# Kernel tuning notes

Measured on AMD Instinct MI355X. Metric: run time of the kernel, lower is better.

The kernel has to match this reference:

```python
import jax, jax.numpy as jnp
import numpy as np

D_MODEL = 256
HIDDEN = 64
R = 1            # corr_radius
MAX_DELTA = 4.0  # max_delta_px
GROUPS = 8       # _gn_groups(64)
B, H, W = 2, 128, 128


def grid_sample_border(img, grid):
    """Bilinear grid_sample, padding_mode='border', align_corners=False.
    img: [B,C,H,W], grid: [B,Hg,Wg,2] (x,y in [-1,1]-ish). -> [B,C,Hg,Wg]"""
    Bi, C, Hi, Wi = img.shape
    x = (grid[..., 0] + 1.0) * (Wi * 0.5) - 0.5
    y = (grid[..., 1] + 1.0) * (Hi * 0.5) - 0.5
    x = jnp.clip(x, 0.0, Wi - 1.0)
    y = jnp.clip(y, 0.0, Hi - 1.0)
    x0 = jnp.floor(x); y0 = jnp.floor(y)
    wx = (x - x0)[:, None]; wy = (y - y0)[:, None]
    x0i = x0.astype(jnp.int32); y0i = y0.astype(jnp.int32)
    x1i = jnp.minimum(x0i + 1, Wi - 1); y1i = jnp.minimum(y0i + 1, Hi - 1)
    imgf = img.reshape(Bi, C, Hi * Wi)
    def gat(im, yi, xi):  # im [C,HW], yi/xi [Hg,Wg]
        return im[:, (yi * Wi + xi).reshape(-1)].reshape(C, *yi.shape)
    g = jax.vmap(gat)
    v00 = g(imgf, y0i, x0i); v01 = g(imgf, y0i, x1i)
    v10 = g(imgf, y1i, x0i); v11 = g(imgf, y1i, x1i)
    return (v00 * (1 - wx) * (1 - wy) + v01 * wx * (1 - wy)
            + v10 * (1 - wx) * wy + v11 * wx * wy)


def l2norm(x, axis):
    n = jnp.sqrt(jnp.sum(x * x, axis=axis, keepdims=True))
    return x / jnp.maximum(n, 1e-12)


def conv2d(x, w, pad):
    return jax.lax.conv_general_dilated(x, w, (1, 1), [(pad, pad), (pad, pad)],
                                        dimension_numbers=('NCHW', 'OIHW', 'NCHW'))


def group_norm(x, gamma, beta, groups=GROUPS, eps=1e-5):
    Bi, C, Hi, Wi = x.shape
    xg = x.reshape(Bi, groups, C // groups, Hi, Wi)
    mu = xg.mean(axis=(2, 3, 4), keepdims=True)
    var = xg.var(axis=(2, 3, 4), keepdims=True)
    xn = ((xg - mu) * jax.lax.rsqrt(var + eps)).reshape(Bi, C, Hi, Wi)
    return xn * gamma[None, :, None, None] + beta[None, :, None, None]


def conv_gn_gelu(x, w, g, b, pad):
    return jax.nn.gelu(group_norm(conv2d(x, w, pad), g, b), approximate=False)


def make_grid(h, w):
    xs = (jnp.arange(w, dtype=jnp.float32) + 0.5) * (2.0 / w) - 1.0
    ys = (jnp.arange(h, dtype=jnp.float32) + 0.5) * (2.0 / h) - 1.0
    gx, gy = jnp.meshgrid(xs, ys, indexing='xy')
    return jnp.stack([gx, gy], axis=-1)[None]  # [1,H,W,2]


def setup_inputs() -> dict:
    key = jax.random.key(0)
    ks = jax.random.split(key, 12)
    in_ch = D_MODEL * 3 + 2 + 1 + (2 * R + 1) ** 2  # 780
    def w(k, o, i, kh, kw):
        return (jax.random.normal(k, (o, i, kh, kw), jnp.float32)
                / np.sqrt(i * kh * kw).astype(np.float32))
    return {
        'feat_A_map': jax.random.normal(ks[0], (B, D_MODEL, H, W), jnp.float32),
        'feat_B_map': jax.random.normal(ks[1], (B, D_MODEL, H, W), jnp.float32),
        'coarse_warp': jax.random.uniform(ks[2], (B, H, W, 2), jnp.float32, -1.0, 1.0),
        'confidence': jax.random.uniform(ks[3], (B, H, W), jnp.float32),
        'enc1_w': w(ks[4], HIDDEN, in_ch, 1, 1),
        'gn1_g': jnp.ones(HIDDEN, jnp.float32), 'gn1_b': jnp.zeros(HIDDEN, jnp.float32),
        'enc2_w': w(ks[5], HIDDEN, HIDDEN, 3, 3),
        'gn2_g': jnp.ones(HIDDEN, jnp.float32), 'gn2_b': jnp.zeros(HIDDEN, jnp.float32),
        'enc3_w': w(ks[6], HIDDEN, HIDDEN, 3, 3),
        'gn3_g': jnp.ones(HIDDEN, jnp.float32), 'gn3_b': jnp.zeros(HIDDEN, jnp.float32),
        'delta_w': w(ks[7], 2, HIDDEN, 3, 3) * 0.01, 'delta_b': jnp.zeros(2, jnp.float32),
        'conf_w': w(ks[8], 1, HIDDEN, 3, 3) * 0.01, 'conf_b': jnp.zeros(1, jnp.float32),
    }


def reference(feat_A_map, feat_B_map, coarse_warp, confidence,
              enc1_w, gn1_g, gn1_b, enc2_w, gn2_g, gn2_b, enc3_w, gn3_g, gn3_b,
              delta_w, delta_b, conf_w, conf_b):
    cw = jnp.clip(jnp.nan_to_num(coarse_warp, nan=0.0, posinf=1.5, neginf=-1.5), -1.5, 1.5)
    route = jax.lax.stop_gradient(cw)  # detached routing warp
    warped_B = grid_sample_border(feat_B_map, route)
    src = make_grid(H, W)
    disp = jnp.transpose(cw - src, (0, 3, 1, 2))  # [B,2,H,W]
    conf = jnp.clip(jnp.nan_to_num(confidence, nan=0.0, posinf=1.0, neginf=0.0), 0.0, 1.0)
    conf_chw = conf[:, None]
    # warp-aware correlation over (2R+1)^2 offsets, vectorized via vmap
    fa_n = l2norm(jnp.nan_to_num(feat_A_map, nan=0.0, posinf=0.0, neginf=0.0), axis=1)
    fb = jnp.nan_to_num(feat_B_map, nan=0.0, posinf=0.0, neginf=0.0)
    offs = jnp.asarray([[2.0 * dx / W, 2.0 * dy / H]
                        for dy in range(-R, R + 1) for dx in range(-R, R + 1)],
                       dtype=jnp.float32)  # [K,2]
    grids = jnp.clip(jnp.nan_to_num(route[None] + offs[:, None, None, None, :],
                                    nan=0.0, posinf=1.5, neginf=-1.5), -1.5, 1.5)
    sampled = jax.vmap(grid_sample_border, in_axes=(None, 0))(fb, grids)  # [K,B,C,H,W]
    corr = jnp.transpose(jnp.sum(fa_n[None] * l2norm(sampled, axis=2), axis=2),
                         (1, 0, 2, 3))  # [B,K,H,W]
    x = jnp.concatenate([feat_A_map, warped_B, jnp.abs(feat_A_map - warped_B),
                         disp, conf_chw, corr], axis=1)
    h = conv_gn_gelu(x, enc1_w, gn1_g, gn1_b, 0)
    h = conv_gn_gelu(h, enc2_w, gn2_g, gn2_b, 1)
    h = conv_gn_gelu(h, enc3_w, gn3_g, gn3_b, 1)
    delta_raw = jnp.transpose(jnp.tanh(conv2d(h, delta_w, 1)
                                       + delta_b[None, :, None, None]), (0, 2, 3, 1))
    scale = jnp.asarray([2.0 * MAX_DELTA / W, 2.0 * MAX_DELTA / H], jnp.float32)
    fine_warp = jnp.clip(jnp.nan_to_num(route + delta_raw * scale,
                                        nan=0.0, posinf=1.5, neginf=-1.5), -1.5, 1.5)
    conf_delta = (conv2d(h, conf_w, 1) + conf_b[None, :, None, None])[:, 0]
    p = jnp.clip(conf, 1e-4, 1.0 - 1e-4)
    base_logit = jnp.log(p) - jnp.log1p(-p)
    refined_logits = base_logit + 0.5 * conf_delta
    refined_conf = jnp.clip(jax.nn.sigmoid(refined_logits), 0.0, 1.0)
    return (fine_warp, refined_conf, refined_logits)
```

## Files before the change

kernel.cpp:

```cpp
#include <hip/hip_runtime.h>
#include <hip/hip_bf16.h>
#include <math.h>

#define B_ 2
#define H_ 128
#define W_ 128
#define C_ 256
#define HID 64
#define PIX_PER (H_*W_)
#define NPIX (B_*PIX_PER)
#define K1STEPS 25
#define K3STEPS 18
#define SROW 264

using f32x4 = __attribute__((ext_vector_type(4))) float;
using s16x8 = __attribute__((ext_vector_type(8))) short;
using u16x2 = __attribute__((ext_vector_type(2))) unsigned short;
using u16x4 = __attribute__((ext_vector_type(4))) unsigned short;
using u16x8 = __attribute__((ext_vector_type(8))) unsigned short;

__device__ __forceinline__ float bf2f(unsigned short u) {
    return __uint_as_float(((unsigned)u) << 16);
}
__device__ __forceinline__ unsigned short f2bf(float f) {
    unsigned u = __float_as_uint(f);
    u += 0x7FFFu + ((u >> 16) & 1u);
    return (unsigned short)(u >> 16);
}
__device__ __forceinline__ float clean15(float v) {
    if (v != v) v = 0.f;
    return fminf(fmaxf(v, -1.5f), 1.5f);
}
__device__ __forceinline__ float clean01(float v) {
    if (v != v) v = 0.f;
    return fminf(fmaxf(v, 0.f), 1.f);
}

__global__ __launch_bounds__(256) void k_transpose(const float* __restrict__ A,
                                                   const float* __restrict__ Bm,
                                                   unsigned short* __restrict__ faT,
                                                   unsigned short* __restrict__ fbT,
                                                   const float* __restrict__ w1,
                                                   const float* __restrict__ w2,
                                                   const float* __restrict__ w3,
                                                   unsigned short* __restrict__ p1,
                                                   unsigned short* __restrict__ p2,
                                                   unsigned short* __restrict__ p3)
{
    if (blockIdx.z == 4) {
        if (blockIdx.y != 0 || blockIdx.x >= 61) return;
        int t = blockIdx.x * 256 + threadIdx.x;
        if (t < 6400) {
            int lane = t & 63, nt = (t >> 6) & 3, ks = t >> 8;
            int n = nt * 16 + (lane & 15);
            int kb = ks * 32 + 8 * (lane >> 4);
#pragma unroll
            for (int j = 0; j < 8; j++) {
                int k = kb + j;
                p1[(size_t)t * 8 + j] = (k < 780) ? f2bf(w1[(size_t)n * 780 + k]) : (unsigned short)0;
            }
        } else if (t < 6400 + 2 * 4608) {
            int which = (t - 6400) / 4608;
            int idx = (t - 6400) % 4608;
            const float* w = which ? w3 : w2;
            unsigned short* p = which ? p3 : p2;
            int lane = idx & 63, nt = (idx >> 6) & 3, ks = idx >> 8;
            int n = nt * 16 + (lane & 15);
            int tap = ks >> 1;
            int ky = tap / 3, kx = tap % 3;
#pragma unroll
            for (int j = 0; j < 8; j++) {
                int c = (ks & 1) * 32 + 8 * (lane >> 4) + j;
                p[(size_t)idx * 8 + j] = f2bf(w[(((size_t)n * 64 + c) * 3 + ky) * 3 + kx]);
            }
        }
        return;
    }
    __shared__ float tile[32][33];
    int hw0 = blockIdx.x * 32;
    int c0  = blockIdx.y * 32;
    int z   = blockIdx.z;
    int b   = z >> 1;
    const float* src = (z & 1) ? Bm : A;
    unsigned short* dst = (z & 1) ? fbT : faT;
    int tx = threadIdx.x & 31, ty = threadIdx.x >> 5;
    const float* s = src + ((size_t)b * C_ + c0) * (size_t)PIX_PER + hw0;
#pragma unroll
    for (int i = 0; i < 32; i += 8) {
        float v = s[(size_t)(ty + i) * PIX_PER + tx];
        if (!isfinite(v)) v = 0.f;
        tile[ty + i][tx] = v;
    }
    __syncthreads();
    unsigned short* d = dst + ((size_t)b * PIX_PER + hw0) * C_ + c0;
    int pr = threadIdx.x & 15;
    int hw = threadIdx.x >> 4;
#pragma unroll
    for (int i = 0; i < 32; i += 16) {
        int hwl = hw + i;
        u16x2 o;
        o[0] = f2bf(tile[2 * pr][hwl]);
        o[1] = f2bf(tile[2 * pr + 1][hwl]);
        *(u16x2*)(d + (size_t)hwl * C_ + 2 * pr) = o;
    }
}

__global__ __launch_bounds__(256) void k_sample(const float* __restrict__ cw,
                                                const float* __restrict__ confp,
                                                const unsigned short* __restrict__ faT,
                                                const unsigned short* __restrict__ fbT,
                                                unsigned short* __restrict__ wbbuf,
                                                unsigned short* __restrict__ tail)
{
    __shared__ unsigned short S[4][17 * SROW];
    __shared__ float CT[4][16 * 20 + 4];
    int lane = threadIdx.x & 63;
    int wv = threadIdx.x >> 6;
    int wid = blockIdx.x * 4 + wv;
    int b = wid >> 14, y = (wid >> 7) & 127, x = wid & 127;

    float gx = clean15(cw[(size_t)wid * 2 + 0]);
    float gy = clean15(cw[(size_t)wid * 2 + 1]);
    float conf = clean01(confp[wid]);

    float pxu = (gx + 1.f) * 64.f - 0.5f;
    float pyu = (gy + 1.f) * 64.f - 0.5f;
    float x0f = floorf(pxu), y0f = floorf(pyu);
    float wx = pxu - x0f, wy = pyu - y0f;
    int x0 = (int)x0f, y0 = (int)y0f;
    int co[4], ro[4];
#pragma unroll
    for (int k = 0; k < 4; k++) {
        co[k] = min(max(x0 - 1 + k, 0), 127) << 8;
        ro[k] = min(max(y0 - 1 + k, 0), 127) << 15;
    }
    const unsigned short* fbP = fbT + ((size_t)b << 22);

    int h = lane >> 5, lo = lane & 31;
    u16x8 stg[8];
#pragma unroll
    for (int i = 0; i < 8; i++) {
        int rr = ro[i >> 1];
        int cc = h ? co[((i & 1) << 1) + 1] : co[(i & 1) << 1];
        stg[i] = *(const u16x8*)(fbP + rr + cc + lo * 8);
    }
    u16x8 stfa;
    if (h == 0) stfa = *(const u16x8*)(faT + (size_t)wid * C_ + lo * 8);

    unsigned short* Sw = &S[wv][0];
#pragma unroll
    for (int i = 0; i < 8; i++)
        *(u16x8*)(Sw + (2 * i + h) * SROW + lo * 8) = stg[i];
    if (h == 0) *(u16x8*)(Sw + 16 * SROW + lo * 8) = stfa;

    int q = lane & 15;
    int tA = (q == 0) ? 16 : q - 1;
    int koff = (lane >> 4) * 8;
    const unsigned short* pA = Sw + tA * SROW + koff;
    const unsigned short* pB = Sw + q * SROW + koff;
    f32x4 acc = {0.f, 0.f, 0.f, 0.f};
#pragma unroll
    for (int ks = 0; ks < 8; ks++) {
        s16x8 av = *(const s16x8*)(pA + ks * 32);
        s16x8 bv = *(const s16x8*)(pB + ks * 32);
        acc = __builtin_amdgcn_mfma_f32_16x16x32_bf16(av, bv, acc, 0, 0, 0);
    }
    *(f32x4*)&CT[wv][q * 20 + (lane >> 4) * 4] = acc;

    float w00 = (1.f - wx) * (1.f - wy), w01 = wx * (1.f - wy);
    float w10 = (1.f - wx) * wy,         w11 = wx * wy;
    u16x4 v5  = *(const u16x4*)(Sw + 5 * SROW + lane * 4);
    u16x4 v6  = *(const u16x4*)(Sw + 6 * SROW + lane * 4);
    u16x4 v9  = *(const u16x4*)(Sw + 9 * SROW + lane * 4);
    u16x4 v10 = *(const u16x4*)(Sw + 10 * SROW + lane * 4);
    u16x4 v15 = *(const u16x4*)(Sw + 15 * SROW + lane * 4);
    u16x4 vfa = *(const u16x4*)(Sw + 16 * SROW + lane * 4);
    float fa2p = 0.f, t152p = 0.f;
    u16x4 wbo;
#pragma unroll
    for (int i = 0; i < 4; i++) {
        float s = w00 * bf2f(v5[i]) + w01 * bf2f(v6[i])
                + w10 * bf2f(v9[i]) + w11 * bf2f(v10[i]);
        wbo[i] = f2bf(s);
        float fv = bf2f(vfa[i]), tv = bf2f(v15[i]);
        fa2p  += fv * fv;
        t152p += tv * tv;
    }
    *(u16x4*)(wbbuf + (size_t)wid * C_ + lane * 4) = wbo;
#pragma unroll
    for (int m = 1; m < 64; m <<= 1) {
        fa2p  += __shfl_xor(fa2p, m);
        t152p += __shfl_xor(t152p, m);
    }

    if (lane < 32) {
        float outv = 0.f;
        if (lane == 0)      outv = gx - (((float)x + 0.5f) * 0.015625f - 1.f);
        else if (lane == 1) outv = gy - (((float)y + 0.5f) * 0.015625f - 1.f);
        else if (lane == 2) outv = conf;
        else if (lane < 12) {
            int j = lane - 3;
            int jd = j / 3, jm = j - jd * 3;
            int m00 = jd * 4 + jm;
            const float* Cw = &CT[wv][0];
            float D00 = Cw[m00 * 20], D01 = Cw[(m00 + 1) * 20];
            float D10 = Cw[(m00 + 4) * 20], D11 = Cw[(m00 + 5) * 20];
            float dot = w00 * D00 + w01 * D01 + w10 * D10 + w11 * D11;
#define GR(a, b) Cw[(b) * 20 + (a) + 1]
            float g11 = (j == 8) ? t152p : GR(m00 + 5, m00 + 5);
            float s2 = w00 * w00 * GR(m00, m00) + w01 * w01 * GR(m00 + 1, m00 + 1)
                     + w10 * w10 * GR(m00 + 4, m00 + 4) + w11 * w11 * g11
                     + 2.f * (w00 * w01 * GR(m00, m00 + 1) + w00 * w10 * GR(m00, m00 + 4)
                            + w00 * w11 * GR(m00, m00 + 5) + w01 * w10 * GR(m00 + 1, m00 + 4)
                            + w01 * w11 * GR(m00 + 1, m00 + 5) + w10 * w11 * GR(m00 + 4, m00 + 5));
#undef GR
            outv = dot * rsqrtf(fmaxf(fa2p, 1e-24f)) * rsqrtf(fmaxf(s2, 1e-24f));
        }
        tail[(size_t)wid * 32 + lane] = f2bf(outv);
    }
}

__device__ __forceinline__ void gn_epilogue(const f32x4 acc[4], float* lds,
                                            float* __restrict__ pbuf, int bid,
                                            int la, int lb, int wv)
{
    int d = la >> 3;
    int slot = wv * 32 + lb * 8 + (la & 7);
#pragma unroll
    for (int nt = 0; nt < 4; nt++) {
        float s  = acc[nt][0] + acc[nt][1] + acc[nt][2] + acc[nt][3];
        float s2 = acc[nt][0] * acc[nt][0] + acc[nt][1] * acc[nt][1]
                 + acc[nt][2] * acc[nt][2] + acc[nt][3] * acc[nt][3];
        int g = nt * 2 + d;
        lds[(g * 128 + slot) * 2 + 0] = s;
        lds[(g * 128 + slot) * 2 + 1] = s2;
    }
    __syncthreads();
    int tid = threadIdx.x;
    int g = tid >> 5, i = tid & 31;
    float s  = lds[(g * 128 + i) * 2]     + lds[(g * 128 + i + 32) * 2]
             + lds[(g * 128 + i + 64) * 2] + lds[(g * 128 + i + 96) * 2];
    float s2 = lds[(g * 128 + i) * 2 + 1]     + lds[(g * 128 + i + 32) * 2 + 1]
             + lds[(g * 128 + i + 64) * 2 + 1] + lds[(g * 128 + i + 96) * 2 + 1];
#pragma unroll
    for (int m = 1; m < 32; m <<= 1) { s += __shfl_xor(s, m); s2 += __shfl_xor(s2, m); }
    if (i == 0) {
        pbuf[(bid * 8 + g) * 2]     = s;
        pbuf[(bid * 8 + g) * 2 + 1] = s2;
    }
}

__global__ __launch_bounds__(256) void k_gemm1(const unsigned short* __restrict__ faT,
                                               const unsigned short* __restrict__ wbbuf,
                                               const unsigned short* __restrict__ tail,
                                               const unsigned short* __restrict__ pack,
                                               unsigned short* __restrict__ hpre,
                                               float* __restrict__ pbuf)
{
    __shared__ float lds[8 * 128 * 2];
    int wave = (blockIdx.x * 256 + threadIdx.x) >> 6;
    int lane = threadIdx.x & 63;
    int la = lane & 15, lb = lane >> 4;
    int row = wave * 16 + la;
    const unsigned short* fa_row = faT   + (size_t)row * C_ + lb * 8;
    const unsigned short* wb_row = wbbuf + (size_t)row * C_ + lb * 8;
    f32x4 acc[4] = {{0,0,0,0},{0,0,0,0},{0,0,0,0},{0,0,0,0}};

#pragma unroll
    for (int ks = 0; ks < 8; ks++) {
        s16x8 a = *(const s16x8*)(fa_row + ks * 32);
#pragma unroll
        for (int nt = 0; nt < 4; nt++)
            acc[nt] = __builtin_amdgcn_mfma_f32_16x16x32_bf16(a,
                *(const s16x8*)(pack + ((size_t)(ks * 4 + nt) * 64 + lane) * 8), acc[nt], 0, 0, 0);
    }
#pragma unroll
    for (int ks = 0; ks < 8; ks++) {
        s16x8 a = *(const s16x8*)(wb_row + ks * 32);
#pragma unroll
        for (int nt = 0; nt < 4; nt++)
            acc[nt] = __builtin_amdgcn_mfma_f32_16x16x32_bf16(a,
                *(const s16x8*)(pack + ((size_t)((ks + 8) * 4 + nt) * 64 + lane) * 8), acc[nt], 0, 0, 0);
    }
#pragma unroll
    for (int ks = 0; ks < 8; ks++) {
        u16x8 av = *(const u16x8*)(fa_row + ks * 32);
        u16x8 bv = *(const u16x8*)(wb_row + ks * 32);
        s16x8 a;
#pragma unroll
        for (int j = 0; j < 8; j++)
            a[j] = (short)f2bf(fabsf(bf2f(av[j]) - bf2f(bv[j])));
#pragma unroll
        for (int nt = 0; nt < 4; nt++)
            acc[nt] = __builtin_amdgcn_mfma_f32_16x16x32_bf16(a,
                *(const s16x8*)(pack + ((size_t)((ks + 16) * 4 + nt) * 64 + lane) * 8), acc[nt], 0, 0, 0);
    }
    {
        s16x8 a = *(const s16x8*)(tail + (size_t)row * 32 + lb * 8);
#pragma unroll
        for (int nt = 0; nt < 4; nt++)
            acc[nt] = __builtin_amdgcn_mfma_f32_16x16x32_bf16(a,
                *(const s16x8*)(pack + ((size_t)(24 * 4 + nt) * 64 + lane) * 8), acc[nt], 0, 0, 0);
    }

    int orow = wave * 16 + lb * 4;
#pragma unroll
    for (int nt = 0; nt < 4; nt++)
#pragma unroll
        for (int r = 0; r < 4; r++)
            hpre[(size_t)(orow + r) * HID + nt * 16 + la] = f2bf(acc[nt][r]);

    gn_epilogue(acc, lds, pbuf, blockIdx.x, la, lb, (threadIdx.x >> 6));
}

__global__ __launch_bounds__(256) void k_conv3(const unsigned short* __restrict__ hin,
                                               const unsigned short* __restrict__ pack,
                                               unsigned short* __restrict__ hpre,
                                               float* __restrict__ pbuf)
{
    __shared__ float lds[8 * 128 * 2];
    int wave = (blockIdx.x * 256 + threadIdx.x) >> 6;
    int lane = threadIdx.x & 63;
    int la = lane & 15, lb = lane >> 4;
    int b = wave >> 10, y = (wave >> 3) & 127, xb = (wave & 7) * 16;
    int xx = xb + la;
    f32x4 acc[4] = {{0,0,0,0},{0,0,0,0},{0,0,0,0},{0,0,0,0}};
#pragma unroll
    for (int ks = 0; ks < K3STEPS; ks++) {
        int tap = ks >> 1;
        int yy = y + tap / 3 - 1;
        int xq = xx + tap % 3 - 1;
        s16x8 a = {0,0,0,0,0,0,0,0};
        if ((unsigned)yy < 128u && (unsigned)xq < 128u)
            a = *(const s16x8*)(hin + ((size_t)((b * 128 + yy) * 128 + xq)) * HID
                                + (ks & 1) * 32 + lb * 8);
#pragma unroll
        for (int nt = 0; nt < 4; nt++)
            acc[nt] = __builtin_amdgcn_mfma_f32_16x16x32_bf16(a,
                *(const s16x8*)(pack + ((size_t)(ks * 4 + nt) * 64 + lane) * 8), acc[nt], 0, 0, 0);
    }
    int orow = wave * 16 + lb * 4;
#pragma unroll
    for (int nt = 0; nt < 4; nt++)
#pragma unroll
        for (int r = 0; r < 4; r++)
            hpre[(size_t)(orow + r) * HID + nt * 16 + la] = f2bf(acc[nt][r]);

    gn_epilogue(acc, lds, pbuf, blockIdx.x, la, lb, (threadIdx.x >> 6));
}

__global__ __launch_bounds__(256) void k_gnapply(const unsigned short* __restrict__ hpre,
                                                 const float* __restrict__ gamma,
                                                 const float* __restrict__ beta,
                                                 const float* __restrict__ pbuf,
                                                 unsigned short* __restrict__ hn)
{
    int pix0 = blockIdx.x * 32;
    int b = pix0 >> 14;
    __shared__ float sm[16];
    {
        int g = threadIdx.x >> 5, i = threadIdx.x & 31;
        float s = 0.f, s2 = 0.f;
#pragma unroll
        for (int k = 0; k < 8; k++) {
            int bid = b * 256 + i + k * 32;
            s  += pbuf[(bid * 8 + g) * 2];
            s2 += pbuf[(bid * 8 + g) * 2 + 1];
        }
#pragma unroll
        for (int m = 1; m < 32; m <<= 1) { s += __shfl_xor(s, m); s2 += __shfl_xor(s2, m); }
        if (i == 0) {
            const float inv = 1.f / 131072.f;
            float mean = s * inv;
            float var = fmaxf(s2 * inv - mean * mean, 0.f);
            sm[g * 2] = mean;
            sm[g * 2 + 1] = rsqrtf(var + 1e-5f);
        }
    }
    __syncthreads();
    int t = blockIdx.x * 256 + threadIdx.x;
    int pix = t >> 3, g = t & 7;
    float mean = sm[g * 2], rstd = sm[g * 2 + 1];
    u16x8 v = *(const u16x8*)(hpre + (size_t)pix * HID + g * 8);
    u16x8 o;
#pragma unroll
    for (int i = 0; i < 8; i++) {
        int c = g * 8 + i;
        float xn = (bf2f(v[i]) - mean) * rstd * gamma[c] + beta[c];
        float ge = 0.5f * xn * (1.f + erff(xn * 0.70710678118654752f));
        o[i] = f2bf(ge);
    }
    *(u16x8*)(hn + (size_t)pix * HID + g * 8) = o;
}

__global__ __launch_bounds__(256) void k_final(const unsigned short* __restrict__ hn,
                                               const float* __restrict__ cw,
                                               const float* __restrict__ confp,
                                               const float* __restrict__ dw,
                                               const float* __restrict__ db,
                                               const float* __restrict__ cwgt,
                                               const float* __restrict__ cb,
                                               float* __restrict__ out)
{
    __shared__ float wds[1154];
    __shared__ float wcs[577];
    int tid = threadIdx.x;
    for (int i = tid; i < 1152; i += 256) wds[i] = dw[i];
    for (int i = tid; i < 576; i += 256) wcs[i] = cwgt[i];
    if (tid == 0) { wds[1152] = db[0]; wds[1153] = db[1]; wcs[576] = cb[0]; }
    __syncthreads();

    int t = blockIdx.x * 256 + tid;
    int pix = t >> 3, part = t & 7;
    int b = pix >> 14, y = (pix >> 7) & 127, x = pix & 127;

    float d0 = 0.f, d1 = 0.f, c0 = 0.f;
#pragma unroll
    for (int ky = 0; ky < 3; ky++) {
        int yy = y + ky - 1;
        if ((unsigned)yy >= 128u) continue;
#pragma unroll
        for (int kx = 0; kx < 3; kx++) {
            int xq = x + kx - 1;
            if ((unsigned)xq >= 128u) continue;
            const unsigned short* hp = hn + (size_t)((b * 128 + yy) * 128 + xq) * HID + part * 8;
            int widx = ky * 3 + kx;
            u16x8 v = *(const u16x8*)hp;
#pragma unroll
            for (int i = 0; i < 8; i++) {
                float f = bf2f(v[i]);
                int c = part * 8 + i;
                d0 += f * wds[c * 9 + widx];
                d1 += f * wds[576 + c * 9 + widx];
                c0 += f * wcs[c * 9 + widx];
            }
        }
    }
#pragma unroll
    for (int m = 1; m < 8; m <<= 1) {
        d0 += __shfl_xor(d0, m);
        d1 += __shfl_xor(d1, m);
        c0 += __shfl_xor(c0, m);
    }
    if (part == 0) {
        d0 = tanhf(d0 + wds[1152]);
        d1 = tanhf(d1 + wds[1153]);
        c0 += wcs[576];

        float gx = clean15(cw[(size_t)pix * 2 + 0]);
        float gy = clean15(cw[(size_t)pix * 2 + 1]);
        float fwx = fminf(fmaxf(gx + d0 * 0.0625f, -1.5f), 1.5f);
        float fwy = fminf(fmaxf(gy + d1 * 0.0625f, -1.5f), 1.5f);

        float conf = clean01(confp[pix]);
        float p = fminf(fmaxf(conf, 1e-4f), 1.f - 1e-4f);
        float bl = logf(p) - log1pf(-p);
        float rl = bl + 0.5f * c0;
        float rc = fminf(fmaxf(1.f / (1.f + expf(-rl)), 0.f), 1.f);

        out[(size_t)pix * 2 + 0] = fwx;
        out[(size_t)pix * 2 + 1] = fwy;
        out[(size_t)NPIX * 2 + pix] = rc;
        out[(size_t)NPIX * 2 + NPIX + pix] = rl;
    }
}

extern "C" void kernel_launch(void* const* d_in, const int* in_sizes, int n_in,
                              void* d_out, int out_size, void* d_ws, size_t ws_size,
                              hipStream_t stream)
{
    const float* feat_A = (const float*)d_in[0];
    const float* feat_B = (const float*)d_in[1];
    const float* cw     = (const float*)d_in[2];
    const float* conf   = (const float*)d_in[3];
    const float* w1     = (const float*)d_in[4];
    const float* g1     = (const float*)d_in[5];
    const float* b1     = (const float*)d_in[6];
    const float* w2     = (const float*)d_in[7];
    const float* g2     = (const float*)d_in[8];
    const float* b2     = (const float*)d_in[9];
    const float* w3     = (const float*)d_in[10];
    const float* g3     = (const float*)d_in[11];
    const float* b3     = (const float*)d_in[12];
    const float* dw     = (const float*)d_in[13];
    const float* db     = (const float*)d_in[14];
    const float* cwgt   = (const float*)d_in[15];
    const float* cb     = (const float*)d_in[16];
    float* out = (float*)d_out;

    char* w = (char*)d_ws;
    size_t o = 0;
    unsigned short* faT  = (unsigned short*)(w + o); o += (size_t)NPIX * C_ * 2;
    unsigned short* fbT  = (unsigned short*)(w + o); o += (size_t)NPIX * C_ * 2;
    unsigned short* wbb  = (unsigned short*)(w + o); o += (size_t)NPIX * C_ * 2;
    unsigned short* tail = (unsigned short*)(w + o); o += (size_t)NPIX * 32 * 2;
    unsigned short* hpre = (unsigned short*)(w + o); o += (size_t)NPIX * HID * 2;
    unsigned short* hnA  = (unsigned short*)(w + o); o += (size_t)NPIX * HID * 2;
    unsigned short* hnB  = (unsigned short*)(w + o); o += (size_t)NPIX * HID * 2;
    unsigned short* p1   = (unsigned short*)(w + o); o += (size_t)K1STEPS * 4 * 64 * 8 * 2;
    unsigned short* p2   = (unsigned short*)(w + o); o += (size_t)K3STEPS * 4 * 64 * 8 * 2;
    unsigned short* p3   = (unsigned short*)(w + o); o += (size_t)K3STEPS * 4 * 64 * 8 * 2;
    float* pbuf = (float*)(w + o);

    k_transpose<<<dim3(PIX_PER / 32, C_ / 32, 5), 256, 0, stream>>>(feat_A, feat_B, faT, fbT,
                                                                    w1, w2, w3, p1, p2, p3);
    k_sample<<<NPIX / 4, 256, 0, stream>>>(cw, conf, faT, fbT, wbb, tail);

    k_gemm1<<<(NPIX / 16) / 4, 256, 0, stream>>>(faT, wbb, tail, p1, hpre, pbuf);
    k_gnapply<<<NPIX / 32, 256, 0, stream>>>(hpre, g1, b1, pbuf, hnA);

    k_conv3<<<(NPIX / 16) / 4, 256, 0, stream>>>(hnA, p2, hpre, pbuf);
    k_gnapply<<<NPIX / 32, 256, 0, stream>>>(hpre, g2, b2, pbuf, hnB);

    k_conv3<<<(NPIX / 16) / 4, 256, 0, stream>>>(hnB, p3, hpre, pbuf);
    k_gnapply<<<NPIX / 32, 256, 0, stream>>>(hpre, g3, b3, pbuf, hnA);

    k_final<<<NPIX * 8 / 256, 256, 0, stream>>>(hnA, cw, conf, dw, db, cwgt, cb, out);
}
```

Baseline: 140.2 us.

## Fuse sampling/correlation kernel with first encoder GEMM through shared memory

Merges the bilinear sampling and correlation kernel with the first 1x1 conv GEMM. Each block now samples 16 pixels (four per wave) and stages the concatenated feature row (feat_A, warped_B, |diff|, tail) in LDS, then runs the GEMM directly from LDS. This removes the global round trip of the warped_B and tail buffers and the separate re-read of feat_A, and computes |diff| once per element. In exchange LDS use per block grows, each wave does four sequential sampling iterations with a block barrier, GN partial sums now come from 1024 blocks per batch (gnapply gets a blocks-per-batch parameter), and the first GEMM is split with one 16-column N tile per wave instead of four per wave.

Measured after the change: 147.9 us. +5.5%, slower.

```diff
diff --git a/kernel.cpp b/kernel.cpp
--- a/kernel.cpp
+++ b/kernel.cpp
@@ -12,6 +12,7 @@
 #define K1STEPS 25
 #define K3STEPS 18
 #define SROW 264
+#define AROW 808
 
 using f32x4 = __attribute__((ext_vector_type(4))) float;
 using s16x8 = __attribute__((ext_vector_type(8))) short;
@@ -105,118 +106,157 @@
     }
 }
 
-__global__ __launch_bounds__(256) void k_sample(const float* __restrict__ cw,
-                                                const float* __restrict__ confp,
-                                                const unsigned short* __restrict__ faT,
-                                                const unsigned short* __restrict__ fbT,
-                                                unsigned short* __restrict__ wbbuf,
-                                                unsigned short* __restrict__ tail)
-{
+__global__ __launch_bounds__(256) void k_samgemm(const float* __restrict__ cw,
+                                                 const float* __restrict__ confp,
+                                                 const unsigned short* __restrict__ faT,
+                                                 const unsigned short* __restrict__ fbT,
+                                                 const unsigned short* __restrict__ pack,
+                                                 unsigned short* __restrict__ hpre,
+                                                 float* __restrict__ pbuf)
+{
+    __shared__ unsigned short Ap[16 * AROW];
     __shared__ unsigned short S[4][17 * SROW];
     __shared__ float CT[4][16 * 20 + 4];
     int lane = threadIdx.x & 63;
     int wv = threadIdx.x >> 6;
-    int wid = blockIdx.x * 4 + wv;
-    int b = wid >> 14, y = (wid >> 7) & 127, x = wid & 127;
-
-    float gx = clean15(cw[(size_t)wid * 2 + 0]);
-    float gy = clean15(cw[(size_t)wid * 2 + 1]);
-    float conf = clean01(confp[wid]);
-
-    float pxu = (gx + 1.f) * 64.f - 0.5f;
-    float pyu = (gy + 1.f) * 64.f - 0.5f;
-    float x0f = floorf(pxu), y0f = floorf(pyu);
-    float wx = pxu - x0f, wy = pyu - y0f;
-    int x0 = (int)x0f, y0 = (int)y0f;
-    int co[4], ro[4];
-#pragma unroll
-    for (int k = 0; k < 4; k++) {
-        co[k] = min(max(x0 - 1 + k, 0), 127) << 8;
-        ro[k] = min(max(y0 - 1 + k, 0), 127) << 15;
-    }
-    const unsigned short* fbP = fbT + ((size_t)b << 22);
-
-    int h = lane >> 5, lo = lane & 31;
-    u16x8 stg[8];
-#pragma unroll
-    for (int i = 0; i < 8; i++) {
-        int rr = ro[i >> 1];
-        int cc = h ? co[((i & 1) << 1) + 1] : co[(i & 1) << 1];
-        stg[i] = *(const u16x8*)(fbP + rr + cc + lo * 8);
-    }
-    u16x8 stfa;
-    if (h == 0) stfa = *(const u16x8*)(faT + (size_t)wid * C_ + lo * 8);
-
     unsigned short* Sw = &S[wv][0];
-#pragma unroll
-    for (int i = 0; i < 8; i++)
-        *(u16x8*)(Sw + (2 * i + h) * SROW + lo * 8) = stg[i];
-    if (h == 0) *(u16x8*)(Sw + 16 * SROW + lo * 8) = stfa;
-
-    int q = lane & 15;
-    int tA = (q == 0) ? 16 : q - 1;
-    int koff = (lane >> 4) * 8;
-    const unsigned short* pA = Sw + tA * SROW + koff;
-    const unsigned short* pB = Sw + q * SROW + koff;
+
+#pragma unroll
+    for (int it = 0; it < 4; it++) {
+        int prow = wv * 4 + it;
+        int wid = blockIdx.x * 16 + prow;
+        int b = wid >> 14, y = (wid >> 7) & 127, x = wid & 127;
+
+        float gx = clean15(cw[(size_t)wid * 2 + 0]);
+        float gy = clean15(cw[(size_t)wid * 2 + 1]);
+        float conf = clean01(confp[wid]);
+
+        float pxu = (gx + 1.f) * 64.f - 0.5f;
+        float pyu = (gy + 1.f) * 64.f - 0.5f;
+        float x0f = floorf(pxu), y0f = floorf(pyu);
+        float wx = pxu - x0f, wy = pyu - y0f;
+        int x0 = (int)x0f, y0 = (int)y0f;
+        int co[4], ro[4];
+#pragma unroll
+        for (int k = 0; k < 4; k++) {
+            co[k] = min(max(x0 - 1 + k, 0), 127) << 8;
+            ro[k] = min(max(y0 - 1 + k, 0), 127) << 15;
+        }
+        const unsigned short* fbP = fbT + ((size_t)b << 22);
+
+        int h = lane >> 5, lo = lane & 31;
+        u16x8 stg[8];
+#pragma unroll
+        for (int i = 0; i < 8; i++) {
+            int rr = ro[i >> 1];
+            int cc = h ? co[((i & 1) << 1) + 1] : co[(i & 1) << 1];
+            stg[i] = *(const u16x8*)(fbP + rr + cc + lo * 8);
+        }
+        u16x8 stfa;
+        if (h == 0) stfa = *(const u16x8*)(faT + (size_t)wid * C_ + lo * 8);
+#pragma unroll
+        for (int i = 0; i < 8; i++)
+            *(u16x8*)(Sw + (2 * i + h) * SROW + lo * 8) = stg[i];
+        if (h == 0) *(u16x8*)(Sw + 16 * SROW + lo * 8) = stfa;
+
+        int q = lane & 15;
+        int tA = (q == 0) ? 16 : q - 1;
+        int koff = (lane >> 4) * 8;
+        const unsigned short* pA = Sw + tA * SROW + koff;
+        const unsigned short* pB = Sw + q * SROW + koff;
+        f32x4 acc = {0.f, 0.f, 0.f, 0.f};
+#pragma unroll
+        for (int ks = 0; ks < 8; ks++) {
+            s16x8 av = *(const s16x8*)(pA + ks * 32);
+            s16x8 bv = *(const s16x8*)(pB + ks * 32);
+            acc = __builtin_amdgcn_mfma_f32_16x16x32_bf16(av, bv, acc, 0, 0, 0);
+        }
+        *(f32x4*)&CT[wv][q * 20 + (lane >> 4) * 4] = acc;
+
+        float w00 = (1.f - wx) * (1.f - wy), w01 = wx * (1.f - wy);
+        float w10 = (1.f - wx) * wy,         w11 = wx * wy;
+        u16x4 v5  = *(const u16x4*)(Sw + 5 * SROW + lane * 4);
+        u16x4 v6  = *(const u16x4*)(Sw + 6 * SROW + lane * 4);
+        u16x4 v9  = *(const u16x4*)(Sw + 9 * SROW + lane * 4);
+        u16x4 v10 = *(const u16x4*)(Sw + 10 * SROW + lane * 4);
+        u16x4 v15 = *(const u16x4*)(Sw + 15 * SROW + lane * 4);
+        u16x4 vfa = *(const u16x4*)(Sw + 16 * SROW + lane * 4);
+        float fa2p = 0.f, t152p = 0.f;
+        u16x4 wbo, dfo;
+#pragma unroll
+        for (int i = 0; i < 4; i++) {
+            float s = w00 * bf2f(v5[i]) + w01 * bf2f(v6[i])
+                    + w10 * bf2f(v9[i]) + w11 * bf2f(v10[i]);
+            float fv = bf2f(vfa[i]), tv = bf2f(v15[i]);
+            wbo[i] = f2bf(s);
+            dfo[i] = f2bf(fabsf(fv - s));
+            fa2p  += fv * fv;
+            t152p += tv * tv;
+        }
+        unsigned short* Ar = &Ap[prow * AROW];
+        *(u16x4*)(Ar + lane * 4)       = vfa;
+        *(u16x4*)(Ar + 256 + lane * 4) = wbo;
+        *(u16x4*)(Ar + 512 + lane * 4) = dfo;
+#pragma unroll
+        for (int m = 1; m < 64; m <<= 1) {
+            fa2p  += __shfl_xor(fa2p, m);
+            t152p += __shfl_xor(t152p, m);
+        }
+
+        if (lane < 32) {
+            float outv = 0.f;
+            if (lane == 0)      outv = gx - (((float)x + 0.5f) * 0.015625f - 1.f);
+            else if (lane == 1) outv = gy - (((float)y + 0.5f) * 0.015625f - 1.f);
+            else if (lane == 2) outv = conf;
+            else if (lane < 12) {
+                int j = lane - 3;
+                int jd = j / 3, jm = j - jd * 3;
+                int m00 = jd * 4 + jm;
+                const float* Cwp = &CT[wv][0];
+                float D00 = Cwp[m00 * 20], D01 = Cwp[(m00 + 1) * 20];
+                float D10 = Cwp[(m00 + 4) * 20], D11 = Cwp[(m00 + 5) * 20];
+                float dot = w00 * D00 + w01 * D01 + w10 * D10 + w11 * D11;
+#define GR(a, b) Cwp[(b) * 20 + (a) + 1]
+                float g11 = (j == 8) ? t152p : GR(m00 + 5, m00 + 5);
+                float s2 = w00 * w00 * GR(m00, m00) + w01 * w01 * GR(m00 + 1, m00 + 1)
+                         + w10 * w10 * GR(m00 + 4, m00 + 4) + w11 * w11 * g11
+                         + 2.f * (w00 * w01 * GR(m00, m00 + 1) + w00 * w10 * GR(m00, m00 + 4)
+                                + w00 * w11 * GR(m00, m00 + 5) + w01 * w10 * GR(m00 + 1, m00 + 4)
+                                + w01 * w11 * GR(m00 + 1, m00 + 5) + w10 * w11 * GR(m00 + 4, m00 + 5));
+#undef GR
+                outv = dot * rsqrtf(fmaxf(fa2p, 1e-24f)) * rsqrtf(fmaxf(s2, 1e-24f));
+            }
+            Ar[768 + lane] = f2bf(outv);
+        }
+    }
+    __syncthreads();
+
+    int la = lane & 15, lb = lane >> 4;
     f32x4 acc = {0.f, 0.f, 0.f, 0.f};
-#pragma unroll
-    for (int ks = 0; ks < 8; ks++) {
-        s16x8 av = *(const s16x8*)(pA + ks * 32);
-        s16x8 bv = *(const s16x8*)(pB + ks * 32);
-        acc = __builtin_amdgcn_mfma_f32_16x16x32_bf16(av, bv, acc, 0, 0, 0);
-    }
-    *(f32x4*)&CT[wv][q * 20 + (lane >> 4) * 4] = acc;
-
-    float w00 = (1.f - wx) * (1.f - wy), w01 = wx * (1.f - wy);
-    float w10 = (1.f - wx) * wy,         w11 = wx * wy;
-    u16x4 v5  = *(const u16x4*)(Sw + 5 * SROW + lane * 4);
-    u16x4 v6  = *(const u16x4*)(Sw + 6 * SROW + lane * 4);
-    u16x4 v9  = *(const u16x4*)(Sw + 9 * SROW + lane * 4);
-    u16x4 v10 = *(const u16x4*)(Sw + 10 * SROW + lane * 4);
-    u16x4 v15 = *(const u16x4*)(Sw + 15 * SROW + lane * 4);
-    u16x4 vfa = *(const u16x4*)(Sw + 16 * SROW + lane * 4);
-    float fa2p = 0.f, t152p = 0.f;
-    u16x4 wbo;
-#pragma unroll
-    for (int i = 0; i < 4; i++) {
-        float s = w00 * bf2f(v5[i]) + w01 * bf2f(v6[i])
-                + w10 * bf2f(v9[i]) + w11 * bf2f(v10[i]);
-        wbo[i] = f2bf(s);
-        float fv = bf2f(vfa[i]), tv = bf2f(v15[i]);
-        fa2p  += fv * fv;
-        t152p += tv * tv;
-    }
-    *(u16x4*)(wbbuf + (size_t)wid * C_ + lane * 4) = wbo;
+    const unsigned short* arow = &Ap[la * AROW + lb * 8];
+#pragma unroll
+    for (int ks = 0; ks < K1STEPS; ks++) {
+        s16x8 a = *(const s16x8*)(arow + ks * 32);
+        s16x8 bv = *(const s16x8*)(pack + ((size_t)(ks * 4 + wv) * 64 + lane) * 8);
+        acc = __builtin_amdgcn_mfma_f32_16x16x32_bf16(a, bv, acc, 0, 0, 0);
+    }
+    int orow = blockIdx.x * 16 + lb * 4;
+#pragma unroll
+    for (int r = 0; r < 4; r++)
+        hpre[(size_t)(orow + r) * HID + wv * 16 + la] = f2bf(acc[r]);
+
+    float s  = acc[0] + acc[1] + acc[2] + acc[3];
+    float s2 = acc[0]*acc[0] + acc[1]*acc[1] + acc[2]*acc[2] + acc[3]*acc[3];
 #pragma unroll
     for (int m = 1; m < 64; m <<= 1) {
-        fa2p  += __shfl_xor(fa2p, m);
-        t152p += __shfl_xor(t152p, m);
-    }
-
-    if (lane < 32) {
-        float outv = 0.f;
-        if (lane == 0)      outv = gx - (((float)x + 0.5f) * 0.015625f - 1.f);
-        else if (lane == 1) outv = gy - (((float)y + 0.5f) * 0.015625f - 1.f);
-        else if (lane == 2) outv = conf;
-        else if (lane < 12) {
-            int j = lane - 3;
-            int jd = j / 3, jm = j - jd * 3;
-            int m00 = jd * 4 + jm;
-            const float* Cw = &CT[wv][0];
-            float D00 = Cw[m00 * 20], D01 = Cw[(m00 + 1) * 20];
-            float D10 = Cw[(m00 + 4) * 20], D11 = Cw[(m00 + 5) * 20];
-            float dot = w00 * D00 + w01 * D01 + w10 * D10 + w11 * D11;
-#define GR(a, b) Cw[(b) * 20 + (a) + 1]
-            float g11 = (j == 8) ? t152p : GR(m00 + 5, m00 + 5);
-            float s2 = w00 * w00 * GR(m00, m00) + w01 * w01 * GR(m00 + 1, m00 + 1)
-                     + w10 * w10 * GR(m00 + 4, m00 + 4) + w11 * w11 * g11
-                     + 2.f * (w00 * w01 * GR(m00, m00 + 1) + w00 * w10 * GR(m00, m00 + 4)
-                            + w00 * w11 * GR(m00, m00 + 5) + w01 * w10 * GR(m00 + 1, m00 + 4)
-                            + w01 * w11 * GR(m00 + 1, m00 + 5) + w10 * w11 * GR(m00 + 4, m00 + 5));
-#undef GR
-            outv = dot * rsqrtf(fmaxf(fa2p, 1e-24f)) * rsqrtf(fmaxf(s2, 1e-24f));
-        }
-        tail[(size_t)wid * 32 + lane] = f2bf(outv);
+        if (m == 8) continue;
+        s  += __shfl_xor(s, m);
+        s2 += __shfl_xor(s2, m);
+    }
+    if (lane == 0 || lane == 8) {
+        int g = wv * 2 + (lane >> 3);
+        pbuf[((size_t)blockIdx.x * 8 + g) * 2]     = s;
+        pbuf[((size_t)blockIdx.x * 8 + g) * 2 + 1] = s2;
     }
 }
 
@@ -248,69 +288,6 @@
         pbuf[(bid * 8 + g) * 2]     = s;
         pbuf[(bid * 8 + g) * 2 + 1] = s2;
     }
-}
-
-__global__ __launch_bounds__(256) void k_gemm1(const unsigned short* __restrict__ faT,
-                                               const unsigned short* __restrict__ wbbuf,
-                                               const unsigned short* __restrict__ tail,
-                                               const unsigned short* __restrict__ pack,
-                                               unsigned short* __restrict__ hpre,
-                                               float* __restrict__ pbuf)
-{
-    __shared__ float lds[8 * 128 * 2];
-    int wave = (blockIdx.x * 256 + threadIdx.x) >> 6;
-    int lane = threadIdx.x & 63;
-    int la = lane & 15, lb = lane >> 4;
-    int row = wave * 16 + la;
-    const unsigned short* fa_row = faT   + (size_t)row * C_ + lb * 8;
-    const unsigned short* wb_row = wbbuf + (size_t)row * C_ + lb * 8;
-    f32x4 acc[4] = {{0,0,0,0},{0,0,0,0},{0,0,0,0},{0,0,0,0}};
-
-#pragma unroll
-    for (int ks = 0; ks < 8; ks++) {
-        s16x8 a = *(const s16x8*)(fa_row + ks * 32);
-#pragma unroll
-        for (int nt = 0; nt < 4; nt++)
-            acc[nt] = __builtin_amdgcn_mfma_f32_16x16x32_bf16(a,
-                *(const s16x8*)(pack + ((size_t)(ks * 4 + nt) * 64 + lane) * 8), acc[nt], 0, 0, 0);
-    }
-#pragma unroll
-    for (int ks = 0; ks < 8; ks++) {
-        s16x8 a = *(const s16x8*)(wb_row + ks * 32);
-#pragma unroll
-        for (int nt = 0; nt < 4; nt++)
-            acc[nt] = __builtin_amdgcn_mfma_f32_16x16x32_bf16(a,
-                *(const s16x8*)(pack + ((size_t)((ks + 8) * 4 + nt) * 64 + lane) * 8), acc[nt], 0, 0, 0);
-    }
-#pragma unroll
-    for (int ks = 0; ks < 8; ks++) {
-        u16x8 av = *(const u16x8*)(fa_row + ks * 32);
-        u16x8 bv = *(const u16x8*)(wb_row + ks * 32);
-        s16x8 a;
-#pragma unroll
-        for (int j = 0; j < 8; j++)
-            a[j] = (short)f2bf(fabsf(bf2f(av[j]) - bf2f(bv[j])));
-#pragma unroll
-        for (int nt = 0; nt < 4; nt++)
-            acc[nt] = __builtin_amdgcn_mfma_f32_16x16x32_bf16(a,
-                *(const s16x8*)(pack + ((size_t)((ks + 16) * 4 + nt) * 64 + lane) * 8), acc[nt], 0, 0, 0);
-    }
-    {
-        s16x8 a = *(const s16x8*)(tail + (size_t)row * 32 + lb * 8);
-#pragma unroll
-        for (int nt = 0; nt < 4; nt++)
-            acc[nt] = __builtin_amdgcn_mfma_f32_16x16x32_bf16(a,
-                *(const s16x8*)(pack + ((size_t)(24 * 4 + nt) * 64 + lane) * 8), acc[nt], 0, 0, 0);
-    }
-
-    int orow = wave * 16 + lb * 4;
-#pragma unroll
-    for (int nt = 0; nt < 4; nt++)
-#pragma unroll
-        for (int r = 0; r < 4; r++)
-            hpre[(size_t)(orow + r) * HID + nt * 16 + la] = f2bf(acc[nt][r]);
-
-    gn_epilogue(acc, lds, pbuf, blockIdx.x, la, lb, (threadIdx.x >> 6));
 }
 
 __global__ __launch_bounds__(256) void k_conv3(const unsigned short* __restrict__ hin,
@@ -353,7 +330,8 @@
                                                  const float* __restrict__ gamma,
                                                  const float* __restrict__ beta,
                                                  const float* __restrict__ pbuf,
-                                                 unsigned short* __restrict__ hn)
+                                                 unsigned short* __restrict__ hn,
+                                                 int bpb)
 {
     int pix0 = blockIdx.x * 32;
     int b = pix0 >> 14;
@@ -361,9 +339,8 @@
     {
         int g = threadIdx.x >> 5, i = threadIdx.x & 31;
         float s = 0.f, s2 = 0.f;
-#pragma unroll
-        for (int k = 0; k < 8; k++) {
-            int bid = b * 256 + i + k * 32;
+        for (int k = 0; k < bpb / 32; k++) {
+            int bid = b * bpb + i + k * 32;
             s  += pbuf[(bid * 8 + g) * 2];
             s2 += pbuf[(bid * 8 + g) * 2 + 1];
         }
@@ -492,8 +469,6 @@
     size_t o = 0;
     unsigned short* faT  = (unsigned short*)(w + o); o += (size_t)NPIX * C_ * 2;
     unsigned short* fbT  = (unsigned short*)(w + o); o += (size_t)NPIX * C_ * 2;
-    unsigned short* wbb  = (unsigned short*)(w + o); o += (size_t)NPIX * C_ * 2;
-    unsigned short* tail = (unsigned short*)(w + o); o += (size_t)NPIX * 32 * 2;
     unsigned short* hpre = (unsigned short*)(w + o); o += (size_t)NPIX * HID * 2;
     unsigned short* hnA  = (unsigned short*)(w + o); o += (size_t)NPIX * HID * 2;
     unsigned short* hnB  = (unsigned short*)(w + o); o += (size_t)NPIX * HID * 2;
@@ -504,16 +479,14 @@
 
     k_transpose<<<dim3(PIX_PER / 32, C_ / 32, 5), 256, 0, stream>>>(feat_A, feat_B, faT, fbT,
                                                                     w1, w2, w3, p1, p2, p3);
-    k_sample<<<NPIX / 4, 256, 0, stream>>>(cw, conf, faT, fbT, wbb, tail);
-
-    k_gemm1<<<(NPIX / 16) / 4, 256, 0, stream>>>(faT, wbb, tail, p1, hpre, pbuf);
-    k_gnapply<<<NPIX / 32, 256, 0, stream>>>(hpre, g1, b1, pbuf, hnA);
+    k_samgemm<<<NPIX / 16, 256, 0, stream>>>(cw, conf, faT, fbT, p1, hpre, pbuf);
+    k_gnapply<<<NPIX / 32, 256, 0, stream>>>(hpre, g1, b1, pbuf, hnA, 1024);
 
     k_conv3<<<(NPIX / 16) / 4, 256, 0, stream>>>(hnA, p2, hpre, pbuf);
-    k_gnapply<<<NPIX / 32, 256, 0, stream>>>(hpre, g2, b2, pbuf, hnB);
+    k_gnapply<<<NPIX / 32, 256, 0, stream>>>(hpre, g2, b2, pbuf, hnB, 256);
 
     k_conv3<<<(NPIX / 16) / 4, 256, 0, stream>>>(hnB, p3, hpre, pbuf);
-    k_gnapply<<<NPIX / 32, 256, 0, stream>>>(hpre, g3, b3, pbuf, hnA);
+    k_gnapply<<<NPIX / 32, 256, 0, stream>>>(hpre, g3, b3, pbuf, hnA, 256);
 
     k_final<<<NPIX * 8 / 256, 256, 0, stream>>>(hnA, cw, conf, dw, db, cwgt, cb, out);
 }
```

## Halve k_sample LDS staging by processing channels in two chunks

Applied to the files above, without the earlier changes.

The sampling kernel now stages the 4x4 neighbourhood plus the A feature row in two 128-channel halves instead of all 256 channels at once. This halves shared memory per wave and lets launch bounds request 6 blocks per CU, aiming for higher occupancy and latency hiding on the gathers. The transpose kernel also writes 4 bf16 per thread instead of 2. In exchange, loads and MFMAs are serialised into two phases with narrower bilinear loads. There is no barrier between a chunk's LDS reads and the next chunk's overwrite, so correctness depends on in-order execution within a single wave.

Result: slower. 190.7 us (+36.0%).

```diff
diff --git a/kernel.cpp b/kernel.cpp
--- a/kernel.cpp
+++ b/kernel.cpp
@@ -11,7 +11,7 @@
 #define NPIX (B_*PIX_PER)
 #define K1STEPS 25
 #define K3STEPS 18
-#define SROW 264
+#define SROW2 132
 
 using f32x4 = __attribute__((ext_vector_type(4))) float;
 using s16x8 = __attribute__((ext_vector_type(8))) short;
@@ -93,26 +93,22 @@
     }
     __syncthreads();
     unsigned short* d = dst + ((size_t)b * PIX_PER + hw0) * C_ + c0;
-    int pr = threadIdx.x & 15;
-    int hw = threadIdx.x >> 4;
-#pragma unroll
-    for (int i = 0; i < 32; i += 16) {
-        int hwl = hw + i;
-        u16x2 o;
-        o[0] = f2bf(tile[2 * pr][hwl]);
-        o[1] = f2bf(tile[2 * pr + 1][hwl]);
-        *(u16x2*)(d + (size_t)hwl * C_ + 2 * pr) = o;
-    }
-}
-
-__global__ __launch_bounds__(256) void k_sample(const float* __restrict__ cw,
-                                                const float* __restrict__ confp,
-                                                const unsigned short* __restrict__ faT,
-                                                const unsigned short* __restrict__ fbT,
-                                                unsigned short* __restrict__ wbbuf,
-                                                unsigned short* __restrict__ tail)
-{
-    __shared__ unsigned short S[4][17 * SROW];
+    int pr = threadIdx.x & 7;
+    int hw = threadIdx.x >> 3;
+    u16x4 o;
+#pragma unroll
+    for (int j = 0; j < 4; j++) o[j] = f2bf(tile[4 * pr + j][hw]);
+    *(u16x4*)(d + (size_t)hw * C_ + 4 * pr) = o;
+}
+
+__global__ __launch_bounds__(256, 6) void k_sample(const float* __restrict__ cw,
+                                                   const float* __restrict__ confp,
+                                                   const unsigned short* __restrict__ faT,
+                                                   const unsigned short* __restrict__ fbT,
+                                                   unsigned short* __restrict__ wbbuf,
+                                                   unsigned short* __restrict__ tail)
+{
+    __shared__ unsigned short S[4][17 * SROW2];
     __shared__ float CT[4][16 * 20 + 4];
     int lane = threadIdx.x & 63;
     int wv = threadIdx.x >> 6;
@@ -136,57 +132,62 @@
     }
     const unsigned short* fbP = fbT + ((size_t)b << 22);
 
-    int h = lane >> 5, lo = lane & 31;
-    u16x8 stg[8];
-#pragma unroll
-    for (int i = 0; i < 8; i++) {
-        int rr = ro[i >> 1];
-        int cc = h ? co[((i & 1) << 1) + 1] : co[(i & 1) << 1];
-        stg[i] = *(const u16x8*)(fbP + rr + cc + lo * 8);
-    }
-    u16x8 stfa;
-    if (h == 0) stfa = *(const u16x8*)(faT + (size_t)wid * C_ + lo * 8);
-
     unsigned short* Sw = &S[wv][0];
-#pragma unroll
-    for (int i = 0; i < 8; i++)
-        *(u16x8*)(Sw + (2 * i + h) * SROW + lo * 8) = stg[i];
-    if (h == 0) *(u16x8*)(Sw + 16 * SROW + lo * 8) = stfa;
-
+    int tl = lane >> 4, cl = lane & 15;
     int q = lane & 15;
     int tA = (q == 0) ? 16 : q - 1;
-    int koff = (lane >> 4) * 8;
-    const unsigned short* pA = Sw + tA * SROW + koff;
-    const unsigned short* pB = Sw + q * SROW + koff;
-    f32x4 acc = {0.f, 0.f, 0.f, 0.f};
-#pragma unroll
-    for (int ks = 0; ks < 8; ks++) {
-        s16x8 av = *(const s16x8*)(pA + ks * 32);
-        s16x8 bv = *(const s16x8*)(pB + ks * 32);
-        acc = __builtin_amdgcn_mfma_f32_16x16x32_bf16(av, bv, acc, 0, 0, 0);
-    }
-    *(f32x4*)&CT[wv][q * 20 + (lane >> 4) * 4] = acc;
+    const unsigned short* pA = Sw + tA * SROW2 + tl * 8;
+    const unsigned short* pB = Sw + q * SROW2 + tl * 8;
 
     float w00 = (1.f - wx) * (1.f - wy), w01 = wx * (1.f - wy);
     float w10 = (1.f - wx) * wy,         w11 = wx * wy;
-    u16x4 v5  = *(const u16x4*)(Sw + 5 * SROW + lane * 4);
-    u16x4 v6  = *(const u16x4*)(Sw + 6 * SROW + lane * 4);
-    u16x4 v9  = *(const u16x4*)(Sw + 9 * SROW + lane * 4);
-    u16x4 v10 = *(const u16x4*)(Sw + 10 * SROW + lane * 4);
-    u16x4 v15 = *(const u16x4*)(Sw + 15 * SROW + lane * 4);
-    u16x4 vfa = *(const u16x4*)(Sw + 16 * SROW + lane * 4);
+    f32x4 acc = {0.f, 0.f, 0.f, 0.f};
     float fa2p = 0.f, t152p = 0.f;
-    u16x4 wbo;
-#pragma unroll
-    for (int i = 0; i < 4; i++) {
-        float s = w00 * bf2f(v5[i]) + w01 * bf2f(v6[i])
-                + w10 * bf2f(v9[i]) + w11 * bf2f(v10[i]);
-        wbo[i] = f2bf(s);
-        float fv = bf2f(vfa[i]), tv = bf2f(v15[i]);
-        fa2p  += fv * fv;
-        t152p += tv * tv;
-    }
-    *(u16x4*)(wbbuf + (size_t)wid * C_ + lane * 4) = wbo;
+
+#pragma unroll
+    for (int c = 0; c < 2; c++) {
+        int cho = c * 128;
+        u16x8 stg[4];
+#pragma unroll
+        for (int i = 0; i < 4; i++) {
+            int t = 4 * i + tl;
+            stg[i] = *(const u16x8*)(fbP + ro[t >> 2] + co[t & 3] + cho + cl * 8);
+        }
+        u16x8 stfa;
+        if (tl == 0) stfa = *(const u16x8*)(faT + (size_t)wid * C_ + cho + cl * 8);
+#pragma unroll
+        for (int i = 0; i < 4; i++)
+            *(u16x8*)(Sw + (4 * i + tl) * SROW2 + cl * 8) = stg[i];
+        if (tl == 0) *(u16x8*)(Sw + 16 * SROW2 + cl * 8) = stfa;
+
+#pragma unroll
+        for (int ks = 0; ks < 4; ks++) {
+            s16x8 av = *(const s16x8*)(pA + ks * 32);
+            s16x8 bv = *(const s16x8*)(pB + ks * 32);
+            acc = __builtin_amdgcn_mfma_f32_16x16x32_bf16(av, bv, acc, 0, 0, 0);
+        }
+
+        u16x2 v5  = *(const u16x2*)(Sw + 5 * SROW2 + lane * 2);
+        u16x2 v6  = *(const u16x2*)(Sw + 6 * SROW2 + lane * 2);
+        u16x2 v9  = *(const u16x2*)(Sw + 9 * SROW2 + lane * 2);
+        u16x2 v10 = *(const u16x2*)(Sw + 10 * SROW2 + lane * 2);
+        u16x2 v15 = *(const u16x2*)(Sw + 15 * SROW2 + lane * 2);
+        u16x2 vfa = *(const u16x2*)(Sw + 16 * SROW2 + lane * 2);
+        u16x2 wbo;
+#pragma unroll
+        for (int i = 0; i < 2; i++) {
+            float s = w00 * bf2f(v5[i]) + w01 * bf2f(v6[i])
+                    + w10 * bf2f(v9[i]) + w11 * bf2f(v10[i]);
+            wbo[i] = f2bf(s);
+            float fv = bf2f(vfa[i]), tv = bf2f(v15[i]);
+            fa2p  += fv * fv;
+            t152p += tv * tv;
+        }
+        *(u16x2*)(wbbuf + (size_t)wid * C_ + cho + lane * 2) = wbo;
+    }
+
+    *(f32x4*)&CT[wv][q * 20 + tl * 4] = acc;
+
 #pragma unroll
     for (int m = 1; m < 64; m <<= 1) {
         fa2p  += __shfl_xor(fa2p, m);
```

## Fuse final GroupNorm+GELU into output conv kernel with LDS halo tiles

Applied to the files above, without the earlier changes.

The last GroupNorm-apply and GELU are merged into the final 3x3 head conv kernel. Each block handles an 8x8 pixel tile, builds a normalized 10x10 halo in shared memory, and then runs the delta and confidence convolutions from LDS. This removes one launch and the global write and read of the normalized hidden buffer, at the cost of recomputing halo pixels and repeating the per-block group-statistics reduction. The transpose store also widens from 2-element to 4-element bf16 writes.

New measurement: 137.3 us, median of 2. 1.02x faster.

```diff
diff --git a/kernel.cpp b/kernel.cpp
--- a/kernel.cpp
+++ b/kernel.cpp
@@ -93,16 +93,12 @@
     }
     __syncthreads();
     unsigned short* d = dst + ((size_t)b * PIX_PER + hw0) * C_ + c0;
-    int pr = threadIdx.x & 15;
-    int hw = threadIdx.x >> 4;
-#pragma unroll
-    for (int i = 0; i < 32; i += 16) {
-        int hwl = hw + i;
-        u16x2 o;
-        o[0] = f2bf(tile[2 * pr][hwl]);
-        o[1] = f2bf(tile[2 * pr + 1][hwl]);
-        *(u16x2*)(d + (size_t)hwl * C_ + 2 * pr) = o;
-    }
+    int pr = threadIdx.x & 7;
+    int hw = threadIdx.x >> 3;
+    u16x4 o;
+#pragma unroll
+    for (int j = 0; j < 4; j++) o[j] = f2bf(tile[4 * pr + j][hw]);
+    *(u16x4*)(d + (size_t)hw * C_ + 4 * pr) = o;
 }
 
 __global__ __launch_bounds__(256) void k_sample(const float* __restrict__ cw,
@@ -393,56 +389,109 @@
     *(u16x8*)(hn + (size_t)pix * HID + g * 8) = o;
 }
 
-__global__ __launch_bounds__(256) void k_final(const unsigned short* __restrict__ hn,
-                                               const float* __restrict__ cw,
-                                               const float* __restrict__ confp,
-                                               const float* __restrict__ dw,
-                                               const float* __restrict__ db,
-                                               const float* __restrict__ cwgt,
-                                               const float* __restrict__ cb,
-                                               float* __restrict__ out)
-{
+__global__ __launch_bounds__(256) void k_gnfinal(const unsigned short* __restrict__ hpre,
+                                                 const float* __restrict__ gamma,
+                                                 const float* __restrict__ beta,
+                                                 const float* __restrict__ pbuf,
+                                                 const float* __restrict__ cw,
+                                                 const float* __restrict__ confp,
+                                                 const float* __restrict__ dw,
+                                                 const float* __restrict__ db,
+                                                 const float* __restrict__ cwgt,
+                                                 const float* __restrict__ cb,
+                                                 float* __restrict__ out)
+{
+    __shared__ unsigned short hnT[100 * 68];
     __shared__ float wds[1154];
     __shared__ float wcs[577];
+    __shared__ float sm[16];
     int tid = threadIdx.x;
+    int bid = blockIdx.x;
+    int b = bid >> 8;
+    int tile = bid & 255;
+    int ty0 = (tile >> 4) << 3, tx0 = (tile & 15) << 3;
+
     for (int i = tid; i < 1152; i += 256) wds[i] = dw[i];
     for (int i = tid; i < 576; i += 256) wcs[i] = cwgt[i];
     if (tid == 0) { wds[1152] = db[0]; wds[1153] = db[1]; wcs[576] = cb[0]; }
+
+    {
+        int g = tid >> 5, i = tid & 31;
+        float s = 0.f, s2 = 0.f;
+#pragma unroll
+        for (int k = 0; k < 8; k++) {
+            int pb = b * 256 + i + k * 32;
+            s  += pbuf[(pb * 8 + g) * 2];
+            s2 += pbuf[(pb * 8 + g) * 2 + 1];
+        }
+#pragma unroll
+        for (int m = 1; m < 32; m <<= 1) { s += __shfl_xor(s, m); s2 += __shfl_xor(s2, m); }
+        if (i == 0) {
+            const float inv = 1.f / 131072.f;
+            float mean = s * inv;
+            float var = fmaxf(s2 * inv - mean * mean, 0.f);
+            sm[g * 2] = mean;
+            sm[g * 2 + 1] = rsqrtf(var + 1e-5f);
+        }
+    }
     __syncthreads();
 
-    int t = blockIdx.x * 256 + tid;
-    int pix = t >> 3, part = t & 7;
-    int b = pix >> 14, y = (pix >> 7) & 127, x = pix & 127;
-
+#pragma unroll
+    for (int pass = 0; pass < 4; pass++) {
+        int idx = pass * 256 + tid;
+        if (idx < 800) {
+            int slot = idx >> 3, c8 = idx & 7;
+            int py = slot / 10, px = slot - py * 10;
+            int gy = ty0 + py - 1, gx = tx0 + px - 1;
+            u16x8 o = {0, 0, 0, 0, 0, 0, 0, 0};
+            if ((unsigned)gy < 128u && (unsigned)gx < 128u) {
+                int gpix = (b << 14) + (gy << 7) + gx;
+                u16x8 v = *(const u16x8*)(hpre + (size_t)gpix * HID + c8 * 8);
+                float mean = sm[c8 * 2], rstd = sm[c8 * 2 + 1];
+#pragma unroll
+                for (int i = 0; i < 8; i++) {
+                    int c = c8 * 8 + i;
+                    float xn = (bf2f(v[i]) - mean) * rstd * gamma[c] + beta[c];
+                    float ge = 0.5f * xn * (1.f + erff(xn * 0.70710678118654752f));
+                    o[i] = f2bf(ge);
+                }
+            }
+            *(u16x8*)(&hnT[slot * 68 + c8 * 8]) = o;
+        }
+    }
+    __syncthreads();
+
+    int p = tid >> 2, part = tid & 3;
+    int py = (p >> 3) + 1, px = (p & 7) + 1;
     float d0 = 0.f, d1 = 0.f, c0 = 0.f;
 #pragma unroll
-    for (int ky = 0; ky < 3; ky++) {
-        int yy = y + ky - 1;
-        if ((unsigned)yy >= 128u) continue;
+    for (int ky = 0; ky < 3; ky++)
 #pragma unroll
         for (int kx = 0; kx < 3; kx++) {
-            int xq = x + kx - 1;
-            if ((unsigned)xq >= 128u) continue;
-            const unsigned short* hp = hn + (size_t)((b * 128 + yy) * 128 + xq) * HID + part * 8;
+            const unsigned short* hp = &hnT[((py + ky - 1) * 10 + (px + kx - 1)) * 68];
             int widx = ky * 3 + kx;
-            u16x8 v = *(const u16x8*)hp;
-#pragma unroll
-            for (int i = 0; i < 8; i++) {
-                float f = bf2f(v[i]);
-                int c = part * 8 + i;
-                d0 += f * wds[c * 9 + widx];
-                d1 += f * wds[576 + c * 9 + widx];
-                c0 += f * wcs[c * 9 + widx];
+#pragma unroll
+            for (int cc = 0; cc < 2; cc++) {
+                int c8 = part * 2 + cc;
+                u16x8 v = *(const u16x8*)(hp + c8 * 8);
+#pragma unroll
+                for (int i = 0; i < 8; i++) {
+                    float f = bf2f(v[i]);
+                    int c = c8 * 8 + i;
+                    d0 += f * wds[c * 9 + widx];
+                    d1 += f * wds[576 + c * 9 + widx];
+                    c0 += f * wcs[c * 9 + widx];
+                }
             }
         }
-    }
-#pragma unroll
-    for (int m = 1; m < 8; m <<= 1) {
+#pragma unroll
+    for (int m = 1; m < 4; m <<= 1) {
         d0 += __shfl_xor(d0, m);
         d1 += __shfl_xor(d1, m);
         c0 += __shfl_xor(c0, m);
     }
     if (part == 0) {
+        int pix = (b << 14) + ((ty0 + py - 1) << 7) + (tx0 + px - 1);
         d0 = tanhf(d0 + wds[1152]);
         d1 = tanhf(d1 + wds[1153]);
         c0 += wcs[576];
@@ -453,8 +502,8 @@
         float fwy = fminf(fmaxf(gy + d1 * 0.0625f, -1.5f), 1.5f);
 
         float conf = clean01(confp[pix]);
-        float p = fminf(fmaxf(conf, 1e-4f), 1.f - 1e-4f);
-        float bl = logf(p) - log1pf(-p);
+        float pp = fminf(fmaxf(conf, 1e-4f), 1.f - 1e-4f);
+        float bl = logf(pp) - log1pf(-pp);
         float rl = bl + 0.5f * c0;
         float rc = fminf(fmaxf(1.f / (1.f + expf(-rl)), 0.f), 1.f);
 
@@ -513,7 +562,6 @@
     k_gnapply<<<NPIX / 32, 256, 0, stream>>>(hpre, g2, b2, pbuf, hnB);
 
     k_conv3<<<(NPIX / 16) / 4, 256, 0, stream>>>(hnB, p3, hpre, pbuf);
-    k_gnapply<<<NPIX / 32, 256, 0, stream>>>(hpre, g3, b3, pbuf, hnA);
-
-    k_final<<<NPIX * 8 / 256, 256, 0, stream>>>(hnA, cw, conf, dw, db, cwgt, cb, out);
-}
+    k_gnfinal<<<512, 256, 0, stream>>>(hpre, g3, b3, pbuf, cw, conf,
+                                       dw, db, cwgt, cb, out);
+}
```
